# Kernel tuning notes

Measured on AMD Instinct MI355X. Metric: run time of the kernel, lower is better.

## Reference

```python
import jax, jax.numpy as jnp
import numpy as np

VOCAB = 100000
EMBED = 256
HIDDEN = 512
H = HIDDEN // 2          # per-direction LSTM hidden
K = 12                   # tagset size
START = 10
STOP = 11
B = 64
T = 512
NEG = -10000.0


def setup_inputs() -> dict:
    key = jax.random.key(0)
    ks = jax.random.split(key, 14)
    s = 1.0 / np.sqrt(H)
    u = lambda k, shape: jax.random.uniform(k, shape, jnp.float32, -s, s)
    transitions = jax.random.normal(ks[12], (K, K), jnp.float32)
    transitions = transitions.at[START, :].set(NEG).at[:, STOP].set(NEG)
    return {
        "sentence": jax.random.randint(ks[0], (B, T), 0, VOCAB),
        "sentence_len": jnp.full((B,), T, dtype=jnp.int32),
        "embed_table": jax.random.normal(ks[1], (VOCAB, EMBED), jnp.float32),
        "Wf_ih": u(ks[2], (4 * H, EMBED)),
        "Wf_hh": u(ks[3], (4 * H, H)),
        "bf_ih": u(ks[4], (4 * H,)),
        "bf_hh": u(ks[5], (4 * H,)),
        "Wb_ih": u(ks[6], (4 * H, EMBED)),
        "Wb_hh": u(ks[7], (4 * H, H)),
        "bb_ih": u(ks[8], (4 * H,)),
        "bb_hh": u(ks[9], (4 * H,)),
        "W_out": u(ks[10], (K, HIDDEN)),
        "b_out": u(ks[11], (K,)),
        "transitions": transitions,
    }


def _lstm_scan(x_proj, W_hh, reverse):
    # x_proj: [T, B, 4H] (input projection + both biases already added)
    def step(carry, xt):
        h, c = carry
        g = xt + h @ W_hh.T
        i, f, gg, o = jnp.split(g, 4, axis=-1)  # torch gate order i,f,g,o
        i = jax.nn.sigmoid(i)
        f = jax.nn.sigmoid(f)
        gg = jnp.tanh(gg)
        o = jax.nn.sigmoid(o)
        c = f * c + i * gg
        h = o * jnp.tanh(c)
        return (h, c), h

    h0 = jnp.zeros((x_proj.shape[1], W_hh.shape[1]), x_proj.dtype)
    _, hs = jax.lax.scan(step, (h0, h0), x_proj, reverse=reverse)
    return hs  # [T, B, H]


def reference(sentence, sentence_len, embed_table,
              Wf_ih, Wf_hh, bf_ih, bf_hh,
              Wb_ih, Wb_hh, bb_ih, bb_hh,
              W_out, b_out, transitions):
    emb = embed_table[sentence]                                   # [B,T,E]
    xf = (jnp.einsum('bte,ge->btg', emb, Wf_ih) + bf_ih + bf_hh).transpose(1, 0, 2)
    xb = (jnp.einsum('bte,ge->btg', emb, Wb_ih) + bb_ih + bb_hh).transpose(1, 0, 2)
    hf = _lstm_scan(xf, Wf_hh, reverse=False)                     # [T,B,H]
    hb = _lstm_scan(xb, Wb_hh, reverse=True)                      # [T,B,H]
    hcat = jnp.concatenate([hf, hb], axis=-1)                     # [T,B,2H]
    feats = jnp.einsum('tbh,kh->tbk', hcat, W_out) + b_out        # [T,B,K]

    nb = sentence.shape[0]
    nt = feats.shape[0]
    kt = transitions.shape[0]
    dp0 = jnp.full((nb, kt), NEG, feats.dtype).at[:, START].set(0.0)
    mask = jnp.arange(nt)[:, None] < sentence_len[None, :]        # [T,B]
    ident = jnp.arange(kt)[None, :]

    def vstep(dp, inp):
        ft, mt = inp                                              # [B,K], [B]
        scores = dp[:, None, :] + transitions[None, :, :]         # [B,Knext,Kprev]
        bptr = jnp.argmax(scores, axis=2)
        dp_new = jnp.max(scores, axis=2) + ft
        dp = jnp.where(mt[:, None], dp_new, dp)
        bptr = jnp.where(mt[:, None], bptr, ident)
        return dp, bptr

    dp, bptrs = jax.lax.scan(vstep, dp0, (feats, mask))           # bptrs: [T,B,K]
    terminal = dp + transitions[STOP][None, :]
    best_last = jnp.argmax(terminal, axis=1)                      # [B]
    path_scores = jnp.max(terminal, axis=1)                       # [B]

    def bstep(tag, bp):
        prev = jnp.take_along_axis(bp, tag[:, None], axis=1)[:, 0]
        return prev, tag

    _, path = jax.lax.scan(bstep, best_last, bptrs, reverse=True)  # [T,B]
    return path_scores, path.transpose(1, 0)
```

## Files before the change

### kernel.cpp

```cpp
#include <hip/hip_runtime.h>
#include <math.h>

#define BATCH 64
#define TLEN 512
#define EMB 256
#define HID 256
#define G4 1024
#define KTAG 12
#define START_TAG 10
#define STOP_TAG 11
#define NEGV -10000.0f
#define SENT 0xFFFFFFFFu

#define LOG2E 1.4426950408889634f

typedef float f4 __attribute__((ext_vector_type(4)));

__device__ __forceinline__ float fsig(float x) {
    return __builtin_amdgcn_rcpf(1.f + __builtin_amdgcn_exp2f(-LOG2E * x));
}
__device__ __forceinline__ float ftanh(float x) {
    return 1.f - 2.f * __builtin_amdgcn_rcpf(1.f + __builtin_amdgcn_exp2f(2.f * LOG2E * x));
}
__device__ __forceinline__ void st_llc(float* p, float v) {
    __hip_atomic_store(p, v, __ATOMIC_RELAXED, __HIP_MEMORY_SCOPE_AGENT);
}
__device__ __forceinline__ unsigned ld_llc_u(const unsigned* p) {
    return __hip_atomic_load(p, __ATOMIC_RELAXED, __HIP_MEMORY_SCOPE_AGENT);
}
__device__ __forceinline__ float red8(float a) {
    float t;
    t = __int_as_float(__builtin_amdgcn_update_dpp(
            0, __float_as_int(a), 0xB1, 0xF, 0xF, true));
    a += t;
    t = __int_as_float(__builtin_amdgcn_update_dpp(
            0, __float_as_int(a), 0x4E, 0xF, 0xF, true));
    a += t;
    t = __int_as_float(__builtin_amdgcn_update_dpp(
            0, __float_as_int(a), 0x141, 0xF, 0xF, true));
    a += t;
    return a;
}

#define MT 128
#define NT 128
#define KC 32
#define LDP 132

__global__ __launch_bounds__(256) void proj_kernel(
    const int* __restrict__ sentence, const float* __restrict__ emb,
    const float* __restrict__ Wf_ih, const float* __restrict__ Wb_ih,
    const float* __restrict__ bf_ih, const float* __restrict__ bf_hh,
    const float* __restrict__ bb_ih, const float* __restrict__ bb_hh,
    float* __restrict__ xf, float* __restrict__ xb) {
    int mtile = blockIdx.x;
    int ntile = blockIdx.y;
    int tid = threadIdx.x;

    __shared__ float As[KC][LDP];
    __shared__ float Bs[KC][LDP];
    __shared__ int tok[MT];

    int g2base = ntile * NT;
    const bool fwd = (g2base < 1024);
    const float* Wih = fwd ? Wf_ih : Wb_ih;
    const float* bia = fwd ? bf_ih : bb_ih;
    const float* bib = fwd ? bf_hh : bb_hh;
    float* dst       = fwd ? xf    : xb;
    int glb = g2base & 1023;

    if (tid < MT) tok[tid] = sentence[(size_t)mtile * MT + tid];
    __syncthreads();

    float acc[8][8];
#pragma unroll
    for (int i = 0; i < 8; ++i)
#pragma unroll
        for (int jj = 0; jj < 8; ++jj) acc[i][jj] = 0.f;

    int m0 = (tid & 15) * 8;
    int n0 = (tid >> 4) * 8;
    int lr = tid >> 3;
    int lk = (tid & 7) * 4;

    for (int k0 = 0; k0 < EMB; k0 += KC) {
#pragma unroll
        for (int i = 0; i < 4; ++i) {
            int r = lr + 32 * i;
            float4 v = *(const float4*)(emb + (size_t)tok[r] * EMB + k0 + lk);
            As[lk + 0][r] = v.x; As[lk + 1][r] = v.y;
            As[lk + 2][r] = v.z; As[lk + 3][r] = v.w;
            float4 w = *(const float4*)(Wih + (size_t)(glb + r) * EMB + k0 + lk);
            Bs[lk + 0][r] = w.x; Bs[lk + 1][r] = w.y;
            Bs[lk + 2][r] = w.z; Bs[lk + 3][r] = w.w;
        }
        __syncthreads();
#pragma unroll
        for (int kk = 0; kk < KC; ++kk) {
            float4 a0 = *(const float4*)&As[kk][m0];
            float4 a1 = *(const float4*)&As[kk][m0 + 4];
            float4 b0 = *(const float4*)&Bs[kk][n0];
            float4 b1 = *(const float4*)&Bs[kk][n0 + 4];
            float av[8] = {a0.x, a0.y, a0.z, a0.w, a1.x, a1.y, a1.z, a1.w};
            float bv[8] = {b0.x, b0.y, b0.z, b0.w, b1.x, b1.y, b1.z, b1.w};
#pragma unroll
            for (int i = 0; i < 8; ++i)
#pragma unroll
                for (int jj = 0; jj < 8; ++jj) acc[i][jj] += av[i] * bv[jj];
        }
        __syncthreads();
    }

    float bs[8];
#pragma unroll
    for (int jj = 0; jj < 8; ++jj) {
        int gl = glb + n0 + jj;
        bs[jj] = bia[gl] + bib[gl];
    }
#pragma unroll
    for (int i = 0; i < 8; ++i) {
        size_t r = (size_t)mtile * MT + m0 + i;
        float4 s0 = {acc[i][0] + bs[0], acc[i][1] + bs[1],
                     acc[i][2] + bs[2], acc[i][3] + bs[3]};
        float4 s1 = {acc[i][4] + bs[4], acc[i][5] + bs[5],
                     acc[i][6] + bs[6], acc[i][7] + bs[7]};
        *(float4*)(dst + r * (size_t)G4 + glb + n0)     = s0;
        *(float4*)(dst + r * (size_t)G4 + glb + n0 + 4) = s1;
    }
}

__global__ __launch_bounds__(256, 1) void lstm_scan12(
    const float* __restrict__ xf, const float* __restrict__ xb,
    const float* __restrict__ Wf_hh, const float* __restrict__ Wb_hh,
    float* __restrict__ hcat) {
    int blk = blockIdx.x;
    int grp = blk & 31;
    int s   = blk >> 5;
    int d   = grp >> 4;
    int gq  = grp & 15;
    int b0  = gq * 4;
    int tid = threadIdx.x;
    int kseg = tid & 7;
    int j    = tid >> 3;
    int J    = s * 32 + j;
    int bown = kseg & 3;

    __shared__ f4 Wl[4][8][256];
    __shared__ float hsL[2][4 * 288];

    const float* Whh = d ? Wb_hh : Wf_hh;
#pragma unroll
    for (int g = 0; g < 4; ++g)
#pragma unroll
        for (int q = 0; q < 8; ++q)
            Wl[g][q][tid] =
                *(const f4*)(Whh + (size_t)(g * 256 + J) * 256 + kseg * 32 + q * 4);

    f4 Wreg[4][8];
#pragma unroll
    for (int g = 0; g < 4; ++g)
#pragma unroll
        for (int q = 0; q < 8; ++q)
            Wreg[g][q] = Wl[g][q][tid];

    const float* x = d ? xb : xf;
    const float* xrow0 = x + (size_t)(b0 + bown) * TLEN * G4 + J;
    int sw = (tid >> 5) * 36 + (tid & 31);
    float c = 0.f;

    const float* xr0 = xrow0 + (size_t)(d ? (TLEN - 1) : 0) * G4;
    float xc0 = xr0[0], xc1 = xr0[256], xc2 = xr0[512], xc3 = xr0[768];

    for (int i = 0; i < TLEN; ++i) {
        int t = d ? (TLEN - 1 - i) : i;
        int buf = i & 1;

        if (i == 0) {
#pragma unroll
            for (int bb = 0; bb < 4; ++bb) hsL[0][bb * 288 + sw] = 0.f;
        } else {
            int tp = d ? (t + 1) : (t - 1);
            const unsigned* base = (const unsigned*)hcat +
                ((size_t)tp * BATCH + b0) * 512 + (size_t)d * HID + tid;
            unsigned u0, u1, u2, u3;
            for (;;) {
                u0 = ld_llc_u(base);
                u1 = ld_llc_u(base + 512);
                u2 = ld_llc_u(base + 1024);
                u3 = ld_llc_u(base + 1536);
                if (u0 != SENT && u1 != SENT && u2 != SENT && u3 != SENT) break;
                __builtin_amdgcn_s_sleep(1);
            }
            hsL[buf][0 * 288 + sw] = __uint_as_float(u0);
            hsL[buf][1 * 288 + sw] = __uint_as_float(u1);
            hsL[buf][2 * 288 + sw] = __uint_as_float(u2);
            hsL[buf][3 * 288 + sw] = __uint_as_float(u3);
        }
        __syncthreads();

        int tn = (i == TLEN - 1) ? t : (d ? (t - 1) : (t + 1));
        const float* xrn = xrow0 + (size_t)tn * G4;
        float xn0 = xrn[0], xn1 = xrn[256], xn2 = xrn[512], xn3 = xrn[768];

        float a[4][4];
#pragma unroll
        for (int g = 0; g < 4; ++g)
#pragma unroll
            for (int bb = 0; bb < 4; ++bb) a[g][bb] = 0.f;

        const float* hbase = hsL[buf] + kseg * 36;
#pragma unroll
        for (int q = 0; q < 8; ++q) {
            f4 w0 = Wreg[0][q];
            f4 w1 = Wreg[1][q];
            f4 w2 = Wreg[2][q];
            f4 w3 = Wreg[3][q];
#pragma unroll
            for (int bb = 0; bb < 4; ++bb) {
                f4 h4 = *(const f4*)(hbase + bb * 288 + q * 4);
                a[0][bb] += w0.x*h4.x + w0.y*h4.y + w0.z*h4.z + w0.w*h4.w;
                a[1][bb] += w1.x*h4.x + w1.y*h4.y + w1.z*h4.z + w1.w*h4.w;
                a[2][bb] += w2.x*h4.x + w2.y*h4.y + w2.z*h4.z + w2.w*h4.w;
                a[3][bb] += w3.x*h4.x + w3.y*h4.y + w3.z*h4.z + w3.w*h4.w;
            }
        }

#pragma unroll
        for (int bb = 0; bb < 4; ++bb) {
            a[0][bb] = red8(a[0][bb]);
            a[1][bb] = red8(a[1][bb]);
            a[2][bb] = red8(a[2][bb]);
            a[3][bb] = red8(a[3][bb]);
        }

        float A0 = bown == 0 ? a[0][0] : bown == 1 ? a[0][1] : bown == 2 ? a[0][2] : a[0][3];
        float A1 = bown == 0 ? a[1][0] : bown == 1 ? a[1][1] : bown == 2 ? a[1][2] : a[1][3];
        float A2 = bown == 0 ? a[2][0] : bown == 1 ? a[2][1] : bown == 2 ? a[2][2] : a[2][3];
        float A3 = bown == 0 ? a[3][0] : bown == 1 ? a[3][1] : bown == 2 ? a[3][2] : a[3][3];

        float ig = fsig(A0 + xc0);
        float fg = fsig(A1 + xc1);
        float gg = ftanh(A2 + xc2);
        float og = fsig(A3 + xc3);
        c = fg * c + ig * gg;
        float h = og * ftanh(c);
        if (kseg < 4)
            st_llc(hcat + ((size_t)t * BATCH + b0 + bown) * 512
                        + (size_t)d * HID + J, h);

        xc0 = xn0; xc1 = xn1; xc2 = xn2; xc3 = xn3;
    }
}

__global__ __launch_bounds__(256) void feats_kernel(
    const float* __restrict__ hcat, const float* __restrict__ Wout,
    const float* __restrict__ bout, float* __restrict__ feats) {
    int wid = threadIdx.x >> 6;
    int lane = threadIdx.x & 63;
    size_t row = (size_t)blockIdx.x * 4 + wid;
    const float* hrow = hcat + row * 512;
    float4 h0 = *(const float4*)(hrow + lane * 8);
    float4 h1 = *(const float4*)(hrow + lane * 8 + 4);
    for (int k2 = 0; k2 < KTAG; ++k2) {
        const float* wr = Wout + (size_t)k2 * 512 + lane * 8;
        float4 w0 = *(const float4*)wr;
        float4 w1 = *(const float4*)(wr + 4);
        float p = h0.x * w0.x + h0.y * w0.y + h0.z * w0.z + h0.w * w0.w
                + h1.x * w1.x + h1.y * w1.y + h1.z * w1.z + h1.w * w1.w;
#pragma unroll
        for (int off = 32; off; off >>= 1) p += __shfl_down(p, off);
        if (lane == 0) feats[row * KTAG + k2] = p + bout[k2];
    }
}

__global__ __launch_bounds__(64) void viterbi_kernel(
    const float* __restrict__ feats, const float* __restrict__ trans,
    const int* __restrict__ slen, float* __restrict__ out) {
    int b = blockIdx.x;
    int lane = threadIdx.x;
    __shared__ unsigned char bp[TLEN][KTAG];

    int len = slen[b];
    float tr[KTAG];
#pragma unroll
    for (int p = 0; p < KTAG; ++p) tr[p] = 0.f;
    if (lane < KTAG) {
#pragma unroll
        for (int p = 0; p < KTAG; ++p) tr[p] = trans[lane * KTAG + p];
    }
    float tstop = (lane < KTAG) ? trans[STOP_TAG * KTAG + lane] : NEGV;
    float dp = (lane == START_TAG) ? 0.f : NEGV;

    float fb[8];
#pragma unroll
    for (int k = 0; k < 8; ++k)
        fb[k] = (lane < KTAG) ? feats[((size_t)k * BATCH + b) * KTAG + lane] : 0.f;

    for (int t0 = 0; t0 < TLEN; t0 += 8) {
#pragma unroll
        for (int u = 0; u < 8; ++u) {
            int t = t0 + u;
            float ftc = fb[u];
            int tn = t + 8;
            fb[u] = (tn < TLEN && lane < KTAG)
                        ? feats[((size_t)tn * BATCH + b) * KTAG + lane] : 0.f;
            float best = -1e30f;
            int arg = 0;
#pragma unroll
            for (int p = 0; p < KTAG; ++p) {
                float dpp = __shfl(dp, p);
                float sc = dpp + tr[p];
                if (sc > best) { best = sc; arg = p; }
            }
            bool m = (t < len);
            if (lane < KTAG) {
                dp = m ? (best + ftc) : dp;
                bp[t][lane] = (unsigned char)(m ? arg : lane);
            }
        }
    }

    float term = dp + tstop;
    float bbest = -1e30f;
    int barg = 0;
#pragma unroll
    for (int p = 0; p < KTAG; ++p) {
        float v = __shfl(term, p);
        if (v > bbest) { bbest = v; barg = p; }
    }
    if (lane == 0) {
        out[b] = bbest;
        float* path = out + BATCH + (size_t)b * TLEN;
        int tag = barg;
        for (int t = TLEN - 1; t >= 0; --t) {
            path[t] = (float)tag;
            tag = bp[t][tag];
        }
    }
}

extern "C" void kernel_launch(void* const* d_in, const int* in_sizes, int n_in,
                              void* d_out, int out_size, void* d_ws, size_t ws_size,
                              hipStream_t stream) {
    const int*   sentence = (const int*)d_in[0];
    const int*   slen     = (const int*)d_in[1];
    const float* emb      = (const float*)d_in[2];
    const float* Wf_ih    = (const float*)d_in[3];
    const float* Wf_hh    = (const float*)d_in[4];
    const float* bf_ih    = (const float*)d_in[5];
    const float* bf_hh    = (const float*)d_in[6];
    const float* Wb_ih    = (const float*)d_in[7];
    const float* Wb_hh    = (const float*)d_in[8];
    const float* bb_ih    = (const float*)d_in[9];
    const float* bb_hh    = (const float*)d_in[10];
    const float* W_out    = (const float*)d_in[11];
    const float* b_out    = (const float*)d_in[12];
    const float* trans    = (const float*)d_in[13];
    float* out = (float*)d_out;

    char* ws = (char*)d_ws;
    float* xf    = (float*)(ws);
    float* xb    = (float*)(ws + 134217728ull);
    float* hcat  = (float*)(ws + 268435456ull);
    float* feats = (float*)(ws + 335544320ull);

    hipMemsetAsync(hcat, 0xFF, 67108864ull, stream);
    hipLaunchKernelGGL(proj_kernel, dim3(256, 16), dim3(256), 0, stream,
                       sentence, emb, Wf_ih, Wb_ih, bf_ih, bf_hh, bb_ih, bb_hh, xf, xb);
    hipLaunchKernelGGL(lstm_scan12, dim3(256), dim3(256), 0, stream,
                       xf, xb, Wf_hh, Wb_hh, hcat);
    hipLaunchKernelGGL(feats_kernel, dim3(8192), dim3(256), 0, stream,
                       hcat, W_out, b_out, feats);
    hipLaunchKernelGGL(viterbi_kernel, dim3(64), dim3(64), 0, stream,
                       feats, trans, slen, out);
}
```

Measured before the change: 2.040 ms.

## Split LSTM recurrence over 512 threads with LDS-resident recurrent weights

The recurrent scan kernel now uses 512 threads per block. Each thread handles a 16-element slice of the hidden dimension instead of 32, and the partial sums are reduced across 16 lanes with an extra DPP step. The recurrent weights are no longer held in registers; they are read from shared memory on every timestep. The aim is to shorten each thread's per-step dot-product chain and relieve register pressure, at the cost of extra LDS traffic on every step of the serial recurrence.

```diff
diff --git a/kernel.cpp b/kernel.cpp
--- a/kernel.cpp
+++ b/kernel.cpp
@@ -28,7 +28,7 @@
 __device__ __forceinline__ unsigned ld_llc_u(const unsigned* p) {
     return __hip_atomic_load(p, __ATOMIC_RELAXED, __HIP_MEMORY_SCOPE_AGENT);
 }
-__device__ __forceinline__ float red8(float a) {
+__device__ __forceinline__ float red16(float a) {
     float t;
     t = __int_as_float(__builtin_amdgcn_update_dpp(
             0, __float_as_int(a), 0xB1, 0xF, 0xF, true));
@@ -39,6 +39,9 @@
     t = __int_as_float(__builtin_amdgcn_update_dpp(
             0, __float_as_int(a), 0x141, 0xF, 0xF, true));
     a += t;
+    t = __int_as_float(__builtin_amdgcn_update_dpp(
+            0, __float_as_int(a), 0x140, 0xF, 0xF, true));
+    a += t;
     return a;
 }
 
@@ -129,7 +132,7 @@
     }
 }
 
-__global__ __launch_bounds__(256, 1) void lstm_scan12(
+__global__ __launch_bounds__(512, 2) void lstm_scan14(
     const float* __restrict__ xf, const float* __restrict__ xb,
     const float* __restrict__ Wf_hh, const float* __restrict__ Wb_hh,
     float* __restrict__ hcat) {
@@ -140,32 +143,26 @@
     int gq  = grp & 15;
     int b0  = gq * 4;
     int tid = threadIdx.x;
-    int kseg = tid & 7;
-    int j    = tid >> 3;
+    int kseg = tid & 15;
+    int j    = tid >> 4;
     int J    = s * 32 + j;
     int bown = kseg & 3;
 
-    __shared__ f4 Wl[4][8][256];
+    __shared__ f4 Wl[4][4][512];
     __shared__ float hsL[2][4 * 288];
 
     const float* Whh = d ? Wb_hh : Wf_hh;
 #pragma unroll
     for (int g = 0; g < 4; ++g)
 #pragma unroll
-        for (int q = 0; q < 8; ++q)
+        for (int q = 0; q < 4; ++q)
             Wl[g][q][tid] =
-                *(const f4*)(Whh + (size_t)(g * 256 + J) * 256 + kseg * 32 + q * 4);
-
-    f4 Wreg[4][8];
-#pragma unroll
-    for (int g = 0; g < 4; ++g)
-#pragma unroll
-        for (int q = 0; q < 8; ++q)
-            Wreg[g][q] = Wl[g][q][tid];
+                *(const f4*)(Whh + (size_t)(g * 256 + J) * 256 + kseg * 16 + q * 4);
 
     const float* x = d ? xb : xf;
     const float* xrow0 = x + (size_t)(b0 + bown) * TLEN * G4 + J;
     int sw = (tid >> 5) * 36 + (tid & 31);
+    int hoff = (kseg >> 1) * 36 + (kseg & 1) * 16;
     float c = 0.f;
 
     const float* xr0 = xrow0 + (size_t)(d ? (TLEN - 1) : 0) * G4;
@@ -175,26 +172,28 @@
         int t = d ? (TLEN - 1 - i) : i;
         int buf = i & 1;
 
-        if (i == 0) {
-#pragma unroll
-            for (int bb = 0; bb < 4; ++bb) hsL[0][bb * 288 + sw] = 0.f;
-        } else {
-            int tp = d ? (t + 1) : (t - 1);
-            const unsigned* base = (const unsigned*)hcat +
-                ((size_t)tp * BATCH + b0) * 512 + (size_t)d * HID + tid;
-            unsigned u0, u1, u2, u3;
-            for (;;) {
-                u0 = ld_llc_u(base);
-                u1 = ld_llc_u(base + 512);
-                u2 = ld_llc_u(base + 1024);
-                u3 = ld_llc_u(base + 1536);
-                if (u0 != SENT && u1 != SENT && u2 != SENT && u3 != SENT) break;
-                __builtin_amdgcn_s_sleep(1);
+        if (tid < 256) {
+            if (i == 0) {
+#pragma unroll
+                for (int bb = 0; bb < 4; ++bb) hsL[0][bb * 288 + sw] = 0.f;
+            } else {
+                int tp = d ? (t + 1) : (t - 1);
+                const unsigned* base = (const unsigned*)hcat +
+                    ((size_t)tp * BATCH + b0) * 512 + (size_t)d * HID + tid;
+                unsigned u0, u1, u2, u3;
+                for (;;) {
+                    u0 = ld_llc_u(base);
+                    u1 = ld_llc_u(base + 512);
+                    u2 = ld_llc_u(base + 1024);
+                    u3 = ld_llc_u(base + 1536);
+                    if (u0 != SENT && u1 != SENT && u2 != SENT && u3 != SENT) break;
+                    __builtin_amdgcn_s_sleep(1);
+                }
+                hsL[buf][0 * 288 + sw] = __uint_as_float(u0);
+                hsL[buf][1 * 288 + sw] = __uint_as_float(u1);
+                hsL[buf][2 * 288 + sw] = __uint_as_float(u2);
+                hsL[buf][3 * 288 + sw] = __uint_as_float(u3);
             }
-            hsL[buf][0 * 288 + sw] = __uint_as_float(u0);
-            hsL[buf][1 * 288 + sw] = __uint_as_float(u1);
-            hsL[buf][2 * 288 + sw] = __uint_as_float(u2);
-            hsL[buf][3 * 288 + sw] = __uint_as_float(u3);
         }
         __syncthreads();
 
@@ -208,13 +207,13 @@
 #pragma unroll
             for (int bb = 0; bb < 4; ++bb) a[g][bb] = 0.f;
 
-        const float* hbase = hsL[buf] + kseg * 36;
-#pragma unroll
-        for (int q = 0; q < 8; ++q) {
-            f4 w0 = Wreg[0][q];
-            f4 w1 = Wreg[1][q];
-            f4 w2 = Wreg[2][q];
-            f4 w3 = Wreg[3][q];
+        const float* hbase = hsL[buf] + hoff;
+#pragma unroll
+        for (int q = 0; q < 4; ++q) {
+            f4 w0 = Wl[0][q][tid];
+            f4 w1 = Wl[1][q][tid];
+            f4 w2 = Wl[2][q][tid];
+            f4 w3 = Wl[3][q][tid];
 #pragma unroll
             for (int bb = 0; bb < 4; ++bb) {
                 f4 h4 = *(const f4*)(hbase + bb * 288 + q * 4);
@@ -227,10 +226,10 @@
 
 #pragma unroll
         for (int bb = 0; bb < 4; ++bb) {
-            a[0][bb] = red8(a[0][bb]);
-            a[1][bb] = red8(a[1][bb]);
-            a[2][bb] = red8(a[2][bb]);
-            a[3][bb] = red8(a[3][bb]);
+            a[0][bb] = red16(a[0][bb]);
+            a[1][bb] = red16(a[1][bb]);
+            a[2][bb] = red16(a[2][bb]);
+            a[3][bb] = red16(a[3][bb]);
         }
 
         float A0 = bown == 0 ? a[0][0] : bown == 1 ? a[0][1] : bown == 2 ? a[0][2] : a[0][3];
@@ -367,7 +366,7 @@
     hipMemsetAsync(hcat, 0xFF, 67108864ull, stream);
     hipLaunchKernelGGL(proj_kernel, dim3(256, 16), dim3(256), 0, stream,
                        sentence, emb, Wf_ih, Wb_ih, bf_ih, bf_hh, bb_ih, bb_hh, xf, xb);
-    hipLaunchKernelGGL(lstm_scan12, dim3(256), dim3(256), 0, stream,
+    hipLaunchKernelGGL(lstm_scan14, dim3(256), dim3(512), 0, stream,
                        xf, xb, Wf_hh, Wb_hh, hcat);
     hipLaunchKernelGGL(feats_kernel, dim3(8192), dim3(256), 0, stream,
                        hcat, W_out, b_out, feats);
```

Measured after the change: 2.217 ms. 8.6% more time.
